# Kernel tuning notes

Hardware: AMD Instinct MI355X
Metric: run time of the kernel (lower is better)

Reference implementation:

```python
import jax, jax.numpy as jnp
import numpy as np

N = 100000
E = 1600000
IN_DIM = 128
HID = 64
HEADS = 1
NEG_SLOPE = 0.2


def setup_inputs() -> dict:
    key = jax.random.key(0)
    ks = jax.random.split(key, 12)
    x = jax.random.normal(ks[0], (N, IN_DIM), dtype=jnp.float32)
    edge_index = jax.random.randint(ks[1], (2, E), 0, N, dtype=jnp.int64)
    s1 = 1.0 / np.sqrt(IN_DIM)
    s2 = 1.0 / np.sqrt(HEADS * HID)
    return {
        "x": x,
        "edge_index": edge_index,
        # layer 1: in_dim -> heads*hid
        "W1": jax.random.normal(ks[2], (IN_DIM, HEADS * HID), dtype=jnp.float32) * s1,
        "a_src1": jax.random.normal(ks[3], (HEADS, HID), dtype=jnp.float32) * s1,
        "a_dst1": jax.random.normal(ks[4], (HEADS, HID), dtype=jnp.float32) * s1,
        "b1": jnp.zeros((HEADS * HID,), dtype=jnp.float32),
        # layer 2: heads*hid -> hid (1 head)
        "W2": jax.random.normal(ks[5], (HEADS * HID, HID), dtype=jnp.float32) * s2,
        "a_src2": jax.random.normal(ks[6], (1, HID), dtype=jnp.float32) * s2,
        "a_dst2": jax.random.normal(ks[7], (1, HID), dtype=jnp.float32) * s2,
        "b2": jnp.zeros((HID,), dtype=jnp.float32),
        # output head
        "W_out": jax.random.normal(ks[8], (HID, 1), dtype=jnp.float32) * (1.0 / np.sqrt(HID)),
        "b_out": jnp.zeros((1,), dtype=jnp.float32),
    }


def _gat_conv(x, src, dst, W, a_src, a_dst, bias, heads, hid):
    n = x.shape[0]
    h = (x @ W).reshape(n, heads, hid)                      # [N, H, D]
    alpha_s = jnp.einsum("nhd,hd->nh", h, a_src)            # [N, H]
    alpha_d = jnp.einsum("nhd,hd->nh", h, a_dst)
    e = alpha_s[src] + alpha_d[dst]                          # [E, H]
    e = jax.nn.leaky_relu(e, NEG_SLOPE)
    # segment softmax over edges sharing the same destination node
    m = jax.ops.segment_max(e, dst, num_segments=n)          # [N, H]
    ex = jnp.exp(e - m[dst])
    denom = jax.ops.segment_sum(ex, dst, num_segments=n)     # [N, H]
    alpha = ex / denom[dst]                                  # [E, H]
    out = jax.ops.segment_sum(h[src] * alpha[:, :, None], dst, num_segments=n)
    return out.reshape(n, heads * hid) + bias


def reference(x, edge_index, W1, a_src1, a_dst1, b1, W2, a_src2, a_dst2, b2, W_out, b_out):
    n = x.shape[0]
    # PyG GATConv default add_self_loops=True
    loops = jnp.arange(n, dtype=edge_index.dtype)
    src = jnp.concatenate([edge_index[0], loops])
    dst = jnp.concatenate([edge_index[1], loops])
    h = jax.nn.elu(_gat_conv(x, src, dst, W1, a_src1, a_dst1, b1, HEADS, HID))
    h = jax.nn.elu(_gat_conv(h, src, dst, W2, a_src2, a_dst2, b2, 1, HID))
    return (h @ W_out + b_out).squeeze(-1)                   # [N]
```

## Files before the change

kernel.cpp:

```cpp
#include <hip/hip_runtime.h>
#include <hip/hip_fp16.h>
#include <math.h>

#define NEG_SLOPE 0.2f
#define BKT_SHIFT 8
#define BKT_NODES (1 << BKT_SHIFT)
#define BKT_CAP 512
#define BKT_FCAP 6144
#define P1_CHUNK 4096

typedef _Float16 f16x8 __attribute__((ext_vector_type(8)));
typedef float    f32x4 __attribute__((ext_vector_type(4)));
union FU  { uint4 u; f16x8 f; };
union H2U { __half2 h; unsigned u; };

__device__ __forceinline__ float lrelu(float x){ return fmaxf(x, NEG_SLOPE * x); }
__device__ __forceinline__ float elu_fast(float x){
  float t = __expf(fminf(x, 0.f)) - 1.f;
  return x > 0.f ? x : t;
}


__global__ __launch_bounds__(256) void k_p1(const int* __restrict__ src, const int* __restrict__ dst,
                                            int E, int B, int* __restrict__ bktCur,
                                            unsigned* __restrict__ pairs,
                                            const float* __restrict__ W1, const float* __restrict__ W2,
                                            uint4* __restrict__ W1f, uint4* __restrict__ W2f){
  __shared__ int h[BKT_CAP], base[BKT_CAP], cur[BKT_CAP];
  int tid = threadIdx.x;
  if (blockIdx.x == 0){
    for (int idx = tid; idx < 16 * 64; idx += 256){
      int lane = idx & 63, fs = idx >> 6;
      int t = fs >> 2, s = fs & 3;
      int m = lane & 15, quad = lane >> 4;
      f16x8 v;
      #pragma unroll
      for (int j = 0; j < 8; ++j)
        v[j] = (_Float16)W1[(s * 32 + quad * 8 + j) * 64 + t * 16 + m];
      FU fu; fu.f = v;
      W1f[fs * 64 + lane] = fu.u;
    }
    for (int idx = tid; idx < 8 * 64; idx += 256){
      int lane = idx & 63, fs = idx >> 6;
      int t = fs >> 1, s = fs & 1;
      int m = lane & 15, quad = lane >> 4;
      f16x8 v;
      #pragma unroll
      for (int j = 0; j < 8; ++j)
        v[j] = (_Float16)W2[(s * 32 + quad * 8 + j) * 64 + t * 16 + m];
      FU fu; fu.f = v;
      W2f[fs * 64 + lane] = fu.u;
    }
  }
  for (int i = tid; i < BKT_CAP; i += 256){ h[i] = 0; cur[i] = 0; }
  __syncthreads();
  int beg = blockIdx.x * P1_CHUNK;
  int end = min(beg + P1_CHUNK, E);
  int m4 = (end - beg) >> 2;
  const int4* d4 = (const int4*)(dst + beg);
  const int4* s4 = (const int4*)(src + beg);
  for (int i = tid; i < m4; i += 256){
    int4 d = d4[i];
    atomicAdd(&h[d.x >> BKT_SHIFT], 1); atomicAdd(&h[d.y >> BKT_SHIFT], 1);
    atomicAdd(&h[d.z >> BKT_SHIFT], 1); atomicAdd(&h[d.w >> BKT_SHIFT], 1);
  }
  for (int i = beg + (m4 << 2) + tid; i < end; i += 256)
    atomicAdd(&h[dst[i] >> BKT_SHIFT], 1);
  __syncthreads();
  for (int i = tid; i < B; i += 256)
    if (h[i]) base[i] = i * BKT_FCAP + atomicAdd(&bktCur[i], h[i]);
  __syncthreads();
  for (int i = tid; i < m4; i += 256){
    int4 d = d4[i]; int4 s = s4[i];
    int b0 = d.x >> BKT_SHIFT, b1 = d.y >> BKT_SHIFT, b2 = d.z >> BKT_SHIFT, b3 = d.w >> BKT_SHIFT;
    int p0 = base[b0] + atomicAdd(&cur[b0], 1);
    pairs[p0] = ((unsigned)(d.x & (BKT_NODES-1)) << 17) | (unsigned)s.x;
    int p1 = base[b1] + atomicAdd(&cur[b1], 1);
    pairs[p1] = ((unsigned)(d.y & (BKT_NODES-1)) << 17) | (unsigned)s.y;
    int p2 = base[b2] + atomicAdd(&cur[b2], 1);
    pairs[p2] = ((unsigned)(d.z & (BKT_NODES-1)) << 17) | (unsigned)s.z;
    int p3 = base[b3] + atomicAdd(&cur[b3], 1);
    pairs[p3] = ((unsigned)(d.w & (BKT_NODES-1)) << 17) | (unsigned)s.w;
  }
  for (int i = beg + (m4 << 2) + tid; i < end; i += 256){
    int d = dst[i], s = src[i];
    int b = d >> BKT_SHIFT;
    int p = base[b] + atomicAdd(&cur[b], 1);
    pairs[p] = ((unsigned)(d & (BKT_NODES-1)) << 17) | (unsigned)s;
  }
}

__global__ __launch_bounds__(256) void k_p2(const unsigned* __restrict__ pairs,
                                            const int* __restrict__ bktCur,
                                            int N, int2* __restrict__ offs2, int* __restrict__ col){
  __shared__ int sc[BKT_NODES], cu[BKT_NODES];
  int b = blockIdx.x, tid = threadIdx.x;
  int nbase = b << BKT_SHIFT;
  int bs = b * BKT_FCAP;
  int be = bs + bktCur[b];
  sc[tid] = 0;
  __syncthreads();
  for (int i = bs + tid; i < be; i += 256)
    atomicAdd(&sc[pairs[i] >> 17], 1);
  __syncthreads();
  int v = sc[tid];
  for (int o = 1; o < 256; o <<= 1){
    int x = (tid >= o) ? sc[tid - o] : 0;
    __syncthreads();
    sc[tid] += x;
    __syncthreads();
  }
  int ex = sc[tid] - v;
  cu[tid] = bs + ex;
  if (nbase + tid < N) offs2[nbase + tid] = make_int2(bs + ex, bs + ex + v);
  __syncthreads();
  for (int i = bs + tid; i < be; i += 256){
    unsigned pr = pairs[i];
    int p = atomicAdd(&cu[pr >> 17], 1);
    col[p] = (int)(pr & 0x1FFFFu);
  }
}

__global__ __launch_bounds__(256) void k_mgemm1(
    const float* __restrict__ X, const uint4* __restrict__ Wf,
    const float* __restrict__ a_src, const float* __restrict__ a_dst,
    uint2* __restrict__ H, float* __restrict__ as_, float* __restrict__ ad_, int n)
{
  int lane = threadIdx.x & 63, wv = threadIdx.x >> 6;
  int quad = lane >> 4, nn = lane & 15;
  int rowb = blockIdx.x * 64 + wv * 16;
  int row = rowb + nn;
  bool ok = row < n;
  int rowc = ok ? row : n - 1;

  f16x8 af[4][4];
  #pragma unroll
  for (int t = 0; t < 4; ++t)
    #pragma unroll
    for (int s = 0; s < 4; ++s){
      FU fu; fu.u = Wf[(t * 4 + s) * 64 + lane];
      af[t][s] = fu.f;
    }

  const float4* Xr = (const float4*)(X + (size_t)rowc * 128);
  float4 xb[4][2];
  #pragma unroll
  for (int s = 0; s < 4; ++s){
    xb[s][0] = Xr[s * 8 + quad * 2];
    xb[s][1] = Xr[s * 8 + quad * 2 + 1];
  }

  f32x4 acc[4] = {};
  #pragma unroll
  for (int s = 0; s < 4; ++s){
    f16x8 bf;
    bf[0] = (_Float16)xb[s][0].x; bf[1] = (_Float16)xb[s][0].y;
    bf[2] = (_Float16)xb[s][0].z; bf[3] = (_Float16)xb[s][0].w;
    bf[4] = (_Float16)xb[s][1].x; bf[5] = (_Float16)xb[s][1].y;
    bf[6] = (_Float16)xb[s][1].z; bf[7] = (_Float16)xb[s][1].w;
    #pragma unroll
    for (int t = 0; t < 4; ++t)
      acc[t] = __builtin_amdgcn_mfma_f32_16x16x32_f16(af[t][s], bf, acc[t], 0, 0, 0);
  }

  if (ok){
    #pragma unroll
    for (int t = 0; t < 4; ++t){
      H2U p0, p1;
      p0.h = __floats2half2_rn(acc[t][0], acc[t][1]);
      p1.h = __floats2half2_rn(acc[t][2], acc[t][3]);
      H[(size_t)row * 16 + t * 4 + quad] = make_uint2(p0.u, p1.u);
    }
  }
  float sl = 0.f, dl = 0.f;
  #pragma unroll
  for (int t = 0; t < 4; ++t){
    float4 a4 = ((const float4*)a_src)[t * 4 + quad];
    float4 d4 = ((const float4*)a_dst)[t * 4 + quad];
    sl += acc[t][0] * a4.x + acc[t][1] * a4.y + acc[t][2] * a4.z + acc[t][3] * a4.w;
    dl += acc[t][0] * d4.x + acc[t][1] * d4.y + acc[t][2] * d4.z + acc[t][3] * d4.w;
  }
  sl += __shfl_xor(sl, 16, 64); sl += __shfl_xor(sl, 32, 64);
  dl += __shfl_xor(dl, 16, 64); dl += __shfl_xor(dl, 32, 64);
  if (lane < 16 && ok){ as_[row] = sl; ad_[row] = dl; }
}

__global__ __launch_bounds__(256) void k_mgemm2(
    const uint4* __restrict__ Xh, const uint4* __restrict__ Wf,
    const float* __restrict__ a_src, const float* __restrict__ a_dst,
    uint2* __restrict__ H, float* __restrict__ as_, float* __restrict__ ad_, int n)
{
  int lane = threadIdx.x & 63, wv = threadIdx.x >> 6;
  int quad = lane >> 4, nn = lane & 15;
  int rowb = blockIdx.x * 64 + wv * 16;
  int row = rowb + nn;
  bool ok = row < n;
  int rowc = ok ? row : n - 1;

  f16x8 af[4][2];
  #pragma unroll
  for (int t = 0; t < 4; ++t)
    #pragma unroll
    for (int s = 0; s < 2; ++s){
      FU fu; fu.u = Wf[(t * 2 + s) * 64 + lane];
      af[t][s] = fu.f;
    }

  f16x8 bf[2];
  #pragma unroll
  for (int s = 0; s < 2; ++s){
    FU fu; fu.u = Xh[(size_t)rowc * 8 + s * 4 + quad];
    bf[s] = fu.f;
  }

  f32x4 acc[4] = {};
  #pragma unroll
  for (int s = 0; s < 2; ++s)
    #pragma unroll
    for (int t = 0; t < 4; ++t)
      acc[t] = __builtin_amdgcn_mfma_f32_16x16x32_f16(af[t][s], bf[s], acc[t], 0, 0, 0);

  if (ok){
    #pragma unroll
    for (int t = 0; t < 4; ++t){
      H2U p0, p1;
      p0.h = __floats2half2_rn(acc[t][0], acc[t][1]);
      p1.h = __floats2half2_rn(acc[t][2], acc[t][3]);
      H[(size_t)row * 16 + t * 4 + quad] = make_uint2(p0.u, p1.u);
    }
  }
  float sl = 0.f, dl = 0.f;
  #pragma unroll
  for (int t = 0; t < 4; ++t){
    float4 a4 = ((const float4*)a_src)[t * 4 + quad];
    float4 d4 = ((const float4*)a_dst)[t * 4 + quad];
    sl += acc[t][0] * a4.x + acc[t][1] * a4.y + acc[t][2] * a4.z + acc[t][3] * a4.w;
    dl += acc[t][0] * d4.x + acc[t][1] * d4.y + acc[t][2] * d4.z + acc[t][3] * d4.w;
  }
  sl += __shfl_xor(sl, 16, 64); sl += __shfl_xor(sl, 32, 64);
  dl += __shfl_xor(dl, 16, 64); dl += __shfl_xor(dl, 32, 64);
  if (lane < 16 && ok){ as_[row] = sl; ad_[row] = dl; }
}

#define FMA8(e, hv) { const __half2* hp = (const __half2*)&(hv);               \
  a[0]=fmaf(e, __half2float(hp[0].x), a[0]); a[1]=fmaf(e, __half2float(hp[0].y), a[1]); \
  a[2]=fmaf(e, __half2float(hp[1].x), a[2]); a[3]=fmaf(e, __half2float(hp[1].y), a[3]); \
  a[4]=fmaf(e, __half2float(hp[2].x), a[4]); a[5]=fmaf(e, __half2float(hp[2].y), a[5]); \
  a[6]=fmaf(e, __half2float(hp[3].x), a[6]); a[7]=fmaf(e, __half2float(hp[3].y), a[7]); }

#define AGG_BODY \
  int lane = threadIdx.x & 63, w = threadIdx.x >> 6;                           \
  int m = lane >> 3, c8 = lane & 7;                                            \
  int node0 = blockIdx.x * 32 + w * 8 + m;                                     \
  bool ok = node0 < n;                                                         \
  int node = ok ? node0 : n - 1;                                               \
  int2 be2 = offs2[node];                                                      \
  int beg = be2.x, d = be2.y - be2.x;                                          \
  int maxd = d;                                                                \
  maxd = max(maxd, __shfl_xor(maxd, 8, 64));                                   \
  maxd = max(maxd, __shfl_xor(maxd, 16, 64));                                  \
  maxd = max(maxd, __shfl_xor(maxd, 32, 64));                                  \
  float adv = ad_[node];                                                       \
  float exs = __expf(lrelu(as_[node] + adv));                                  \
  uint4 hself = H4[(size_t)node * 8 + c8];                                     \
  float denom = exs;                                                           \
  float a[8];                                                                  \
  { const __half2* hp = (const __half2*)&hself;                                \
    _Pragma("unroll")                                                          \
    for (int i = 0; i < 4; ++i){                                               \
      a[2*i]   = exs * __half2float(hp[i].x);                                  \
      a[2*i+1] = exs * __half2float(hp[i].y);                                  \
    } }                                                                        \
  for (int j = 0; j < maxd; j += 4){                                           \
    int ss[4]; float asv[4]; uint4 hv[4];                                      \
    _Pragma("unroll")                                                          \
    for (int u = 0; u < 4; ++u) ss[u] = (j + u < d) ? col[beg + j + u] : 0;    \
    _Pragma("unroll")                                                          \
    for (int u = 0; u < 4; ++u) asv[u] = as_[ss[u]];                           \
    _Pragma("unroll")                                                          \
    for (int u = 0; u < 4; ++u) hv[u] = H4[(size_t)ss[u] * 8 + c8];            \
    _Pragma("unroll")                                                          \
    for (int u = 0; u < 4; ++u){                                               \
      float e = (j + u < d) ? __expf(lrelu(asv[u] + adv)) : 0.f;               \
      denom += e;                                                              \
      FMA8(e, hv[u])                                                           \
    }                                                                          \
  }

__global__ __launch_bounds__(256) void k_agg1(
    const int2* __restrict__ offs2, const int* __restrict__ col,
    const uint4* __restrict__ H4, const float* __restrict__ as_, const float* __restrict__ ad_,
    const float* __restrict__ bias, uint4* __restrict__ outH, int n)
{
  AGG_BODY
  float inv = 1.f / denom;
  float4 b0 = *(const float4*)&bias[8 * c8];
  float4 b1 = *(const float4*)&bias[8 * c8 + 4];
  float bb[8] = {b0.x, b0.y, b0.z, b0.w, b1.x, b1.y, b1.z, b1.w};
  unsigned oh[4];
  #pragma unroll
  for (int i = 0; i < 4; ++i){
    float v0 = elu_fast(fmaf(a[2*i],   inv, bb[2*i]));
    float v1 = elu_fast(fmaf(a[2*i+1], inv, bb[2*i+1]));
    __half2 h = __floats2half2_rn(v0, v1);
    oh[i] = *(unsigned*)&h;
  }
  if (ok){
    uint4 ov; ov.x = oh[0]; ov.y = oh[1]; ov.z = oh[2]; ov.w = oh[3];
    outH[(size_t)node * 8 + c8] = ov;
  }
}

__global__ __launch_bounds__(256) void k_agg2(
    const int2* __restrict__ offs2, const int* __restrict__ col,
    const uint4* __restrict__ H4, const float* __restrict__ as_, const float* __restrict__ ad_,
    const float* __restrict__ bias, const float* __restrict__ Wout, const float* __restrict__ bout,
    float* __restrict__ out, int n)
{
  AGG_BODY
  float inv = 1.f / denom;
  float4 b0 = *(const float4*)&bias[8 * c8];
  float4 b1 = *(const float4*)&bias[8 * c8 + 4];
  float4 w0 = *(const float4*)&Wout[8 * c8];
  float4 w1 = *(const float4*)&Wout[8 * c8 + 4];
  float bb[8] = {b0.x, b0.y, b0.z, b0.w, b1.x, b1.y, b1.z, b1.w};
  float ww[8] = {w0.x, w0.y, w0.z, w0.w, w1.x, w1.y, w1.z, w1.w};
  float p = 0.f;
  #pragma unroll
  for (int i = 0; i < 8; ++i)
    p += elu_fast(fmaf(a[i], inv, bb[i])) * ww[i];
  p += __shfl_xor(p, 1, 64); p += __shfl_xor(p, 2, 64); p += __shfl_xor(p, 4, 64);
  if (c8 == 0 && ok) out[node] = p + bout[0];
}

extern "C" void kernel_launch(void* const* d_in, const int* in_sizes, int n_in,
                              void* d_out, int out_size, void* d_ws, size_t ws_size,
                              hipStream_t stream)
{
  const float* x    = (const float*)d_in[0];
  const int*   ei   = (const int*)d_in[1];
  const float* W1   = (const float*)d_in[2];
  const float* as1w = (const float*)d_in[3];
  const float* ad1w = (const float*)d_in[4];
  const float* b1   = (const float*)d_in[5];
  const float* W2   = (const float*)d_in[6];
  const float* as2w = (const float*)d_in[7];
  const float* ad2w = (const float*)d_in[8];
  const float* b2   = (const float*)d_in[9];
  const float* Wout = (const float*)d_in[10];
  const float* bout = (const float*)d_in[11];
  float* out = (float*)d_out;

  const int N = in_sizes[0] / 128;
  const int E = in_sizes[1] / 2;
  const int* srcA = ei;
  const int* dstA = ei + E;
  const int B = (N + BKT_NODES - 1) >> BKT_SHIFT;

  char* p = (char*)d_ws;
  auto alloc = [&](size_t bytes){ char* r = p; p += (bytes + 255) & ~255ull; return r; };
  int*   bktCur = (int*)alloc(BKT_CAP * 4);
  int2*  offs2  = (int2*)alloc((size_t)N * 8);
  int*   col    = (int*)alloc((size_t)B * BKT_FCAP * 4);
  float* vas1 = (float*)alloc((size_t)N * 4);
  float* vad1 = (float*)alloc((size_t)N * 4);
  float* vas2 = (float*)alloc((size_t)N * 4);
  float* vad2 = (float*)alloc((size_t)N * 4);
  uint4* w1f  = (uint4*)alloc(16 * 64 * 16);
  uint4* w2f  = (uint4*)alloc(8 * 64 * 16);
  uint2* h1   = (uint2*)alloc((size_t)N * 64 * 2);
  uint2* h1e  = (uint2*)alloc((size_t)N * 64 * 2);
  unsigned* pairs = (unsigned*)h1;
  uint2* h2   = h1;

  hipMemsetAsync(bktCur, 0, BKT_CAP * 4, stream);

  int nchunk = (E + P1_CHUNK - 1) / P1_CHUNK;
  k_p1<<<nchunk, 256, 0, stream>>>(srcA, dstA, E, B, bktCur, pairs, W1, W2, w1f, w2f);
  k_p2<<<B, 256, 0, stream>>>(pairs, bktCur, N, offs2, col);

  int gblocks = (N + 63) / 64;
  k_mgemm1<<<gblocks, 256, 0, stream>>>(x, w1f, as1w, ad1w, h1, vas1, vad1, N);
  k_agg1  <<<(N + 31) / 32, 256, 0, stream>>>(offs2, col, (const uint4*)h1, vas1, vad1, b1, (uint4*)h1e, N);
  k_mgemm2<<<gblocks, 256, 0, stream>>>((const uint4*)h1e, w2f, as2w, ad2w, h2, vas2, vad2, N);
  k_agg2  <<<(N + 31) / 32, 256, 0, stream>>>(offs2, col, (const uint4*)h2, vas2, vad2, b2, Wout, bout, out, N);
}
```

Baseline: 242.7 us.

## Fuse edge bucketing pass with layer-1 GEMM; use nontemporal gathers in aggregation

```diff
diff --git a/kernel.cpp b/kernel.cpp
--- a/kernel.cpp
+++ b/kernel.cpp
@@ -11,6 +11,7 @@
 
 typedef _Float16 f16x8 __attribute__((ext_vector_type(8)));
 typedef float    f32x4 __attribute__((ext_vector_type(4)));
+typedef unsigned u32x4 __attribute__((ext_vector_type(4)));
 union FU  { uint4 u; f16x8 f; };
 union H2U { __half2 h; unsigned u; };
 
@@ -19,27 +20,85 @@
   float t = __expf(fminf(x, 0.f)) - 1.f;
   return x > 0.f ? x : t;
 }
-
-
-__global__ __launch_bounds__(256) void k_p1(const int* __restrict__ src, const int* __restrict__ dst,
-                                            int E, int B, int* __restrict__ bktCur,
-                                            unsigned* __restrict__ pairs,
-                                            const float* __restrict__ W1, const float* __restrict__ W2,
-                                            uint4* __restrict__ W1f, uint4* __restrict__ W2f){
+__device__ __forceinline__ uint4 ntload4(const uint4* p){
+  u32x4 v = __builtin_nontemporal_load((const u32x4*)p);
+  uint4 r; r.x = v.x; r.y = v.y; r.z = v.z; r.w = v.w; return r;
+}
+
+__global__ __launch_bounds__(256) void k_fused1(
+    const int* __restrict__ src, const int* __restrict__ dst, int E, int B, int nchunk,
+    int* __restrict__ bktCur, unsigned* __restrict__ pairs,
+    const float* __restrict__ W1, const float* __restrict__ W2, uint4* __restrict__ W2f,
+    const float* __restrict__ X, const float* __restrict__ a_src, const float* __restrict__ a_dst,
+    uint2* __restrict__ H, float* __restrict__ as_, float* __restrict__ ad_, int n)
+{
+  int tid = threadIdx.x;
+  if (blockIdx.x >= nchunk){
+    int bid = blockIdx.x - nchunk;
+    int lane = tid & 63, wv = tid >> 6;
+    int quad = lane >> 4, nn = lane & 15;
+    int row = bid * 64 + wv * 16 + nn;
+    bool ok = row < n;
+    int rowc = ok ? row : n - 1;
+
+    f16x8 af[4][4];
+    #pragma unroll
+    for (int t = 0; t < 4; ++t)
+      #pragma unroll
+      for (int s = 0; s < 4; ++s){
+        f16x8 v;
+        #pragma unroll
+        for (int j = 0; j < 8; ++j)
+          v[j] = (_Float16)W1[(s * 32 + quad * 8 + j) * 64 + t * 16 + nn];
+        af[t][s] = v;
+      }
+
+    const float4* Xr = (const float4*)(X + (size_t)rowc * 128);
+    float4 xb[4][2];
+    #pragma unroll
+    for (int s = 0; s < 4; ++s){
+      xb[s][0] = Xr[s * 8 + quad * 2];
+      xb[s][1] = Xr[s * 8 + quad * 2 + 1];
+    }
+
+    f32x4 acc[4] = {};
+    #pragma unroll
+    for (int s = 0; s < 4; ++s){
+      f16x8 bf;
+      bf[0] = (_Float16)xb[s][0].x; bf[1] = (_Float16)xb[s][0].y;
+      bf[2] = (_Float16)xb[s][0].z; bf[3] = (_Float16)xb[s][0].w;
+      bf[4] = (_Float16)xb[s][1].x; bf[5] = (_Float16)xb[s][1].y;
+      bf[6] = (_Float16)xb[s][1].z; bf[7] = (_Float16)xb[s][1].w;
+      #pragma unroll
+      for (int t = 0; t < 4; ++t)
+        acc[t] = __builtin_amdgcn_mfma_f32_16x16x32_f16(af[t][s], bf, acc[t], 0, 0, 0);
+    }
+
+    if (ok){
+      #pragma unroll
+      for (int t = 0; t < 4; ++t){
+        H2U p0, p1;
+        p0.h = __floats2half2_rn(acc[t][0], acc[t][1]);
+        p1.h = __floats2half2_rn(acc[t][2], acc[t][3]);
+        H[(size_t)row * 16 + t * 4 + quad] = make_uint2(p0.u, p1.u);
+      }
+    }
+    float sl = 0.f, dl = 0.f;
+    #pragma unroll
+    for (int t = 0; t < 4; ++t){
+      float4 a4 = ((const float4*)a_src)[t * 4 + quad];
+      float4 d4 = ((const float4*)a_dst)[t * 4 + quad];
+      sl += acc[t][0] * a4.x + acc[t][1] * a4.y + acc[t][2] * a4.z + acc[t][3] * a4.w;
+      dl += acc[t][0] * d4.x + acc[t][1] * d4.y + acc[t][2] * d4.z + acc[t][3] * d4.w;
+    }
+    sl += __shfl_xor(sl, 16, 64); sl += __shfl_xor(sl, 32, 64);
+    dl += __shfl_xor(dl, 16, 64); dl += __shfl_xor(dl, 32, 64);
+    if (lane < 16 && ok){ as_[row] = sl; ad_[row] = dl; }
+    return;
+  }
+
   __shared__ int h[BKT_CAP], base[BKT_CAP], cur[BKT_CAP];
-  int tid = threadIdx.x;
   if (blockIdx.x == 0){
-    for (int idx = tid; idx < 16 * 64; idx += 256){
-      int lane = idx & 63, fs = idx >> 6;
-      int t = fs >> 2, s = fs & 3;
-      int m = lane & 15, quad = lane >> 4;
-      f16x8 v;
-      #pragma unroll
-      for (int j = 0; j < 8; ++j)
-        v[j] = (_Float16)W1[(s * 32 + quad * 8 + j) * 64 + t * 16 + m];
-      FU fu; fu.f = v;
-      W1f[fs * 64 + lane] = fu.u;
-    }
     for (int idx = tid; idx < 8 * 64; idx += 256){
       int lane = idx & 63, fs = idx >> 6;
       int t = fs >> 1, s = fs & 1;
@@ -119,70 +178,6 @@
     int p = atomicAdd(&cu[pr >> 17], 1);
     col[p] = (int)(pr & 0x1FFFFu);
   }
-}
-
-__global__ __launch_bounds__(256) void k_mgemm1(
-    const float* __restrict__ X, const uint4* __restrict__ Wf,
-    const float* __restrict__ a_src, const float* __restrict__ a_dst,
-    uint2* __restrict__ H, float* __restrict__ as_, float* __restrict__ ad_, int n)
-{
-  int lane = threadIdx.x & 63, wv = threadIdx.x >> 6;
-  int quad = lane >> 4, nn = lane & 15;
-  int rowb = blockIdx.x * 64 + wv * 16;
-  int row = rowb + nn;
-  bool ok = row < n;
-  int rowc = ok ? row : n - 1;
-
-  f16x8 af[4][4];
-  #pragma unroll
-  for (int t = 0; t < 4; ++t)
-    #pragma unroll
-    for (int s = 0; s < 4; ++s){
-      FU fu; fu.u = Wf[(t * 4 + s) * 64 + lane];
-      af[t][s] = fu.f;
-    }
-
-  const float4* Xr = (const float4*)(X + (size_t)rowc * 128);
-  float4 xb[4][2];
-  #pragma unroll
-  for (int s = 0; s < 4; ++s){
-    xb[s][0] = Xr[s * 8 + quad * 2];
-    xb[s][1] = Xr[s * 8 + quad * 2 + 1];
-  }
-
-  f32x4 acc[4] = {};
-  #pragma unroll
-  for (int s = 0; s < 4; ++s){
-    f16x8 bf;
-    bf[0] = (_Float16)xb[s][0].x; bf[1] = (_Float16)xb[s][0].y;
-    bf[2] = (_Float16)xb[s][0].z; bf[3] = (_Float16)xb[s][0].w;
-    bf[4] = (_Float16)xb[s][1].x; bf[5] = (_Float16)xb[s][1].y;
-    bf[6] = (_Float16)xb[s][1].z; bf[7] = (_Float16)xb[s][1].w;
-    #pragma unroll
-    for (int t = 0; t < 4; ++t)
-      acc[t] = __builtin_amdgcn_mfma_f32_16x16x32_f16(af[t][s], bf, acc[t], 0, 0, 0);
-  }
-
-  if (ok){
-    #pragma unroll
-    for (int t = 0; t < 4; ++t){
-      H2U p0, p1;
-      p0.h = __floats2half2_rn(acc[t][0], acc[t][1]);
-      p1.h = __floats2half2_rn(acc[t][2], acc[t][3]);
-      H[(size_t)row * 16 + t * 4 + quad] = make_uint2(p0.u, p1.u);
-    }
-  }
-  float sl = 0.f, dl = 0.f;
-  #pragma unroll
-  for (int t = 0; t < 4; ++t){
-    float4 a4 = ((const float4*)a_src)[t * 4 + quad];
-    float4 d4 = ((const float4*)a_dst)[t * 4 + quad];
-    sl += acc[t][0] * a4.x + acc[t][1] * a4.y + acc[t][2] * a4.z + acc[t][3] * a4.w;
-    dl += acc[t][0] * d4.x + acc[t][1] * d4.y + acc[t][2] * d4.z + acc[t][3] * d4.w;
-  }
-  sl += __shfl_xor(sl, 16, 64); sl += __shfl_xor(sl, 32, 64);
-  dl += __shfl_xor(dl, 16, 64); dl += __shfl_xor(dl, 32, 64);
-  if (lane < 16 && ok){ as_[row] = sl; ad_[row] = dl; }
 }
 
 __global__ __launch_bounds__(256) void k_mgemm2(
@@ -262,7 +257,7 @@
   maxd = max(maxd, __shfl_xor(maxd, 32, 64));                                  \
   float adv = ad_[node];                                                       \
   float exs = __expf(lrelu(as_[node] + adv));                                  \
-  uint4 hself = H4[(size_t)node * 8 + c8];                                     \
+  uint4 hself = ntload4(&H4[(size_t)node * 8 + c8]);                           \
   float denom = exs;                                                           \
   float a[8];                                                                  \
   { const __half2* hp = (const __half2*)&hself;                                \
@@ -278,7 +273,7 @@
     _Pragma("unroll")                                                          \
     for (int u = 0; u < 4; ++u) asv[u] = as_[ss[u]];                           \
     _Pragma("unroll")                                                          \
-    for (int u = 0; u < 4; ++u) hv[u] = H4[(size_t)ss[u] * 8 + c8];            \
+    for (int u = 0; u < 4; ++u) hv[u] = ntload4(&H4[(size_t)ss[u] * 8 + c8]);  \
     _Pragma("unroll")                                                          \
     for (int u = 0; u < 4; ++u){                                               \
       float e = (j + u < d) ? __expf(lrelu(asv[u] + adv)) : 0.f;               \
@@ -366,21 +361,19 @@
   float* vad1 = (float*)alloc((size_t)N * 4);
   float* vas2 = (float*)alloc((size_t)N * 4);
   float* vad2 = (float*)alloc((size_t)N * 4);
-  uint4* w1f  = (uint4*)alloc(16 * 64 * 16);
   uint4* w2f  = (uint4*)alloc(8 * 64 * 16);
   uint2* h1   = (uint2*)alloc((size_t)N * 64 * 2);
   uint2* h1e  = (uint2*)alloc((size_t)N * 64 * 2);
-  unsigned* pairs = (unsigned*)h1;
+  unsigned* pairs = (unsigned*)alloc((size_t)B * BKT_FCAP * 4);
   uint2* h2   = h1;
 
   hipMemsetAsync(bktCur, 0, BKT_CAP * 4, stream);
 
   int nchunk = (E + P1_CHUNK - 1) / P1_CHUNK;
-  k_p1<<<nchunk, 256, 0, stream>>>(srcA, dstA, E, B, bktCur, pairs, W1, W2, w1f, w2f);
-  k_p2<<<B, 256, 0, stream>>>(pairs, bktCur, N, offs2, col);
-
   int gblocks = (N + 63) / 64;
-  k_mgemm1<<<gblocks, 256, 0, stream>>>(x, w1f, as1w, ad1w, h1, vas1, vad1, N);
+  k_fused1<<<nchunk + gblocks, 256, 0, stream>>>(srcA, dstA, E, B, nchunk, bktCur, pairs,
+                                                 W1, W2, w2f, x, as1w, ad1w, h1, vas1, vad1, N);
+  k_p2    <<<B, 256, 0, stream>>>(pairs, bktCur, N, offs2, col);
   k_agg1  <<<(N + 31) / 32, 256, 0, stream>>>(offs2, col, (const uint4*)h1, vas1, vad1, b1, (uint4*)h1e, N);
   k_mgemm2<<<gblocks, 256, 0, stream>>>((const uint4*)h1e, w2f, as2w, ad2w, h2, vas2, vad2, N);
   k_agg2  <<<(N + 31) / 32, 256, 0, stream>>>(offs2, col, (const uint4*)h2, vas2, vad2, b2, Wout, bout, out, N);
```

After: 289.7 us. 1.19x slower.
